# Kernel optimization log

Measured on AMD Instinct MI355X. Metric: run time of the kernel, lower is better.

Reference implementation:

```python
import jax, jax.numpy as jnp
import numpy as np

# Baked genome DAG structure (static per-instance in the original module)
N_IN = 256
LAYER_SIZES = [256, 256, 256, 256, 64]  # 4 hidden layers + output layer
N_OUT = LAYER_SIZES[-1]
N_EVAL = sum(LAYER_SIZES)  # 1088 eval nodes (node_evals)
DEG = 32                   # incoming links per eval node
BATCH = 8192


def setup_inputs() -> dict:
    key = jax.random.key(0)
    kx, kw, kb, kr = jax.random.split(key, 4)
    x = jax.random.normal(kx, (BATCH, N_IN), dtype=jnp.float32)
    # connection weights, node bias, node response (learned genome params)
    w = jax.random.normal(kw, (N_EVAL, DEG), dtype=jnp.float32) * 0.5
    bias = jax.random.normal(kb, (N_EVAL,), dtype=jnp.float32) * 0.1
    response = 1.0 + jax.random.normal(kr, (N_EVAL,), dtype=jnp.float32) * 0.1
    # per-layer source indices: each eval node connects to DEG earlier nodes
    src_rows = []
    offset = N_IN  # number of nodes topologically before current layer
    for li, sz in enumerate(LAYER_SIZES):
        ks = jax.random.fold_in(key, 100 + li)
        src_rows.append(jax.random.randint(ks, (sz, DEG), 0, offset, dtype=jnp.int32))
        offset += sz
    src_idx = jnp.concatenate(src_rows, axis=0)  # [N_EVAL, DEG]
    return {"x": x, "w": w, "bias": bias, "response": response, "src_idx": src_idx}


def reference(x, w, bias, response, src_idx):
    # values: [B, n_nodes_so_far]; starts as the input node values
    values = x
    row = 0
    for sz in LAYER_SIZES:  # small fixed structural loop (topological layers)
        s = src_idx[row:row + sz]                       # [sz, DEG]
        gathered = values[:, s]                         # [B, sz, DEG]
        agg = jnp.einsum('bsd,sd->bs', gathered, w[row:row + sz])  # sum aggregation
        out = jax.nn.relu(bias[row:row + sz] + response[row:row + sz] * agg)
        values = jnp.concatenate([values, out], axis=1)
        row += sz
    return values[:, -N_OUT:]  # [B, N_OUT]
```

## Files before the change

### kernel.cpp

```cpp
#include <hip/hip_runtime.h>

#define N_IN    256
#define N_EVAL  1088
#define TOTALW  1344
#define DEG     32
#define TILE_B  16
#define NTHREADS 256

__device__ __forceinline__ int gbyte(int c, int h) {
    return ((c << 5) + (h << 4)) ^ (int)((((unsigned)c >> 2) & 7u) << 5);
}

__device__ __forceinline__ unsigned int bf16rne2(float lo, float hi) {
    unsigned int ul = __float_as_uint(lo);
    unsigned int uh = __float_as_uint(hi);
    ul = (ul + 0x7fffu + ((ul >> 16) & 1u)) >> 16;
    uh = (uh + 0x7fffu + ((uh >> 16) & 1u)) & 0xffff0000u;
    return ul | uh;
}

__device__ __forceinline__ void fmadw(unsigned int d, float wv, float* acc) {
    acc[0] = fmaf(__uint_as_float(d << 16), wv, acc[0]);
    acc[1] = fmaf(__uint_as_float(d & 0xffff0000u), wv, acc[1]);
}

__device__ __forceinline__ void colacc16(const unsigned int* vals, int c, float wv,
                                         float* acc) {
    const uint4* p = (const uint4*)((const char*)vals + gbyte(c, 0));
    uint4 a = p[0];
    uint4 b = p[1];
    fmadw(a.x, wv, acc + 0);  fmadw(a.y, wv, acc + 2);
    fmadw(a.z, wv, acc + 4);  fmadw(a.w, wv, acc + 6);
    fmadw(b.x, wv, acc + 8);  fmadw(b.y, wv, acc + 10);
    fmadw(b.z, wv, acc + 12); fmadw(b.w, wv, acc + 14);
}

__global__ __launch_bounds__(NTHREADS) void neat_eval(
    const float* __restrict__ x, const float* __restrict__ w,
    const float* __restrict__ bias, const float* __restrict__ resp,
    const int* __restrict__ src, float* __restrict__ out)
{
    __shared__ unsigned int vals[TOTALW * 8];
    const int tid = threadIdx.x;
    const int b0  = blockIdx.x * TILE_B;

    #pragma unroll
    for (int i = 0; i < 2; ++i) {
        int g = tid + i * NTHREADS;
        int c = g & 255;
        int h = g >> 8;
        unsigned int pk[4];
        #pragma unroll
        for (int j = 0; j < 4; ++j) {
            float lo = x[(size_t)(b0 + h * 8 + 2 * j    ) * N_IN + c];
            float hi = x[(size_t)(b0 + h * 8 + 2 * j + 1) * N_IN + c];
            pk[j] = bf16rne2(lo, hi);
        }
        *(uint4*)((char*)vals + gbyte(c, h)) = make_uint4(pk[0], pk[1], pk[2], pk[3]);
    }
    __syncthreads();

    int row = 0, outoff = N_IN;
    #pragma unroll
    for (int li = 0; li < 5; ++li) {
        const int sz = (li < 4) ? 256 : 64;
        for (int n = tid; n < sz; n += NTHREADS) {
            const int gr = row + n;
            const int4*   s4 = (const int4*)(src + (size_t)gr * DEG);
            const float4* w4 = (const float4*)(w   + (size_t)gr * DEG);
            float acc[16];
            #pragma unroll
            for (int i = 0; i < 16; ++i) acc[i] = 0.f;
            #pragma unroll
            for (int k = 0; k < DEG / 4; ++k) {
                int4   i4 = s4[k];
                float4 wv = w4[k];
                colacc16(vals, i4.x, wv.x, acc);
                colacc16(vals, i4.y, wv.y, acc);
                colacc16(vals, i4.z, wv.z, acc);
                colacc16(vals, i4.w, wv.w, acc);
            }
            const float bb = bias[gr], rr = resp[gr];
            unsigned int pk[8];
            #pragma unroll
            for (int j = 0; j < 8; ++j) {
                float lo = fmaxf(fmaf(rr, acc[2 * j    ], bb), 0.f);
                float hi = fmaxf(fmaf(rr, acc[2 * j + 1], bb), 0.f);
                pk[j] = bf16rne2(lo, hi);
            }
            int ob = gbyte(outoff + n, 0);
            *(uint4*)((char*)vals + ob)      = make_uint4(pk[0], pk[1], pk[2], pk[3]);
            *(uint4*)((char*)vals + ob + 16) = make_uint4(pk[4], pk[5], pk[6], pk[7]);
        }
        __syncthreads();
        row += sz; outoff += sz;
    }

    #pragma unroll
    for (int i = 0; i < 4; ++i) {
        int idx = tid + i * NTHREADS;
        int c = idx & 63;
        int b = idx >> 6;
        int col = TOTALW - 64 + c;
        const unsigned int* g =
            (const unsigned int*)((const char*)vals + gbyte(col, b >> 3));
        unsigned int d = g[(b & 7) >> 1];
        float v = (b & 1) ? __uint_as_float(d & 0xffff0000u)
                          : __uint_as_float(d << 16);
        out[(size_t)(b0 + b) * 64 + c] = v;
    }
}

extern "C" void kernel_launch(void* const* d_in, const int* in_sizes, int n_in,
                              void* d_out, int out_size, void* d_ws, size_t ws_size,
                              hipStream_t stream) {
    const float* x    = (const float*)d_in[0];
    const float* w    = (const float*)d_in[1];
    const float* bias = (const float*)d_in[2];
    const float* resp = (const float*)d_in[3];
    const int*   src  = (const int*)d_in[4];
    float* out = (float*)d_out;

    const int batch = in_sizes[0] / N_IN;
    const int grid  = batch / TILE_B;
    neat_eval<<<grid, NTHREADS, 0, stream>>>(x, w, bias, resp, src, out);
}
```

Baseline: 30.32 us.

## Densify sparse genome weights and evaluate layers with bf16 MFMA

Adds a preprocessing kernel that scatters each node's 32 sparse weighted links into a dense bf16 weight matrix laid out in MFMA fragment order, merging duplicate sources. The main kernel then computes each layer as a dense GEMM over all earlier nodes with 16x16x32 bf16 MFMA, 32 batch rows per block and activations kept in swizzled LDS. This replaces scalar gather-FMA work with matrix-core work, at the cost of far more FLOPs (dense over up to 1280 columns), a memset plus an extra kernel launch each call, and reading a roughly 1.5 MB weight buffer. The old scalar kernel remains as a fallback when the workspace is too small.

Result: slower. 57.99 us (+91.3%).

```diff
diff --git a/kernel.cpp b/kernel.cpp
--- a/kernel.cpp
+++ b/kernel.cpp
@@ -1,70 +1,235 @@
 #include <hip/hip_runtime.h>
 
-#define N_IN    256
-#define N_EVAL  1088
-#define TOTALW  1344
-#define DEG     32
-#define TILE_B  16
-#define NTHREADS 256
-
-__device__ __forceinline__ int gbyte(int c, int h) {
-    return ((c << 5) + (h << 4)) ^ (int)((((unsigned)c >> 2) & 7u) << 5);
-}
-
-__device__ __forceinline__ unsigned int bf16rne2(float lo, float hi) {
-    unsigned int ul = __float_as_uint(lo);
-    unsigned int uh = __float_as_uint(hi);
+#define N_IN   256
+#define N_EVAL 1088
+#define TOTALW 1344
+#define DEG    32
+
+typedef __attribute__((ext_vector_type(8))) short short8;
+typedef __attribute__((ext_vector_type(4))) float f32x4;
+typedef unsigned short u16;
+typedef unsigned int   u32;
+
+__device__ __forceinline__ u32 pk2(float lo, float hi) {
+    u32 ul = __float_as_uint(lo);
+    u32 uh = __float_as_uint(hi);
     ul = (ul + 0x7fffu + ((ul >> 16) & 1u)) >> 16;
     uh = (uh + 0x7fffu + ((uh >> 16) & 1u)) & 0xffff0000u;
     return ul | uh;
 }
-
-__device__ __forceinline__ void fmadw(unsigned int d, float wv, float* acc) {
+__device__ __forceinline__ u16 bf1(float v) {
+    u32 u = __float_as_uint(v);
+    return (u16)((u + 0x7fffu + ((u >> 16) & 1u)) >> 16);
+}
+
+__global__ __launch_bounds__(256) void build_m(
+    const int* __restrict__ src, const float* __restrict__ w,
+    u16* __restrict__ B)
+{
+    int gn = blockIdx.x * 256 + threadIdx.x;
+    if (gn >= N_EVAL) return;
+    const int li   = gn >> 8;
+    const int nloc = gn & 255;
+    const int NT   = (li < 4) ? 16 : 4;
+    const int loff[5] = {0, 65536, 196608, 393216, 655360};
+    const int base = loff[li];
+
+    int c[DEG]; float ow[DEG];
+    const int4*   s4 = (const int4*)(src + (size_t)gn * DEG);
+    const float4* w4 = (const float4*)(w   + (size_t)gn * DEG);
+    #pragma unroll
+    for (int k = 0; k < 8; ++k) {
+        int4 ci = s4[k]; float4 wf = w4[k];
+        c[4*k+0]=ci.x; c[4*k+1]=ci.y; c[4*k+2]=ci.z; c[4*k+3]=ci.w;
+        ow[4*k+0]=wf.x; ow[4*k+1]=wf.y; ow[4*k+2]=wf.z; ow[4*k+3]=wf.w;
+    }
+    float acc[DEG]; bool live[DEG];
+    #pragma unroll
+    for (int d = 0; d < DEG; ++d) {
+        float s = 0.f;
+        #pragma unroll
+        for (int d2 = 0; d2 < DEG; ++d2)
+            if (d2 <= d && c[d2] == c[d]) s += ow[d2];
+        acc[d] = s;
+        bool lv = true;
+        #pragma unroll
+        for (int d2 = 0; d2 < DEG; ++d2)
+            if (d2 > d && c[d2] == c[d]) lv = false;
+        live[d] = lv;
+    }
+    const int nt = nloc >> 4, ln = nloc & 15;
+    #pragma unroll
+    for (int d = 0; d < DEG; ++d) {
+        if (!live[d]) continue;
+        int cc = c[d];
+        int kt = cc >> 5, ko = cc & 31;
+        int lane = ((ko >> 3) << 4) | ln;
+        int idx = base + ((kt * NT + nt) * 64 + lane) * 8 + (ko & 7);
+        B[idx] = bf1(acc[d]);
+    }
+}
+
+#define TILE_B 32
+#define RSTRIDE (TOTALW * 2)
+
+__global__ __launch_bounds__(512) void neat_mfma(
+    const float* __restrict__ x, const u16* __restrict__ Bbuf,
+    const float* __restrict__ bias, const float* __restrict__ resp,
+    float* __restrict__ out)
+{
+    __shared__ uint4 ldsq[(TILE_B * RSTRIDE) / 16];
+    char* lds = (char*)ldsq;
+    const int tid  = threadIdx.x;
+    const int b0   = blockIdx.x * TILE_B;
+    const int lane = tid & 63;
+    const int wvid = tid >> 6;
+
+    #pragma unroll
+    for (int i = 0; i < 4; ++i) {
+        int f4 = tid + i * 512;
+        int row = f4 >> 6;
+        int c4  = f4 & 63;
+        float4 xv = ((const float4*)(x + (size_t)(b0 + row) * N_IN))[c4];
+        u32 p0 = pk2(xv.x, xv.y), p1 = pk2(xv.z, xv.w);
+        int byte = row * RSTRIDE + ((c4 * 8) ^ ((row & 7) << 4));
+        *(u32*)(lds + byte)     = p0;
+        *(u32*)(lds + byte + 4) = p1;
+    }
+    __syncthreads();
+
+    const short8* Bf = (const short8*)Bbuf;
+    const int r0  = lane & 15;
+    const int r1  = r0 + 16;
+    const int g16 = (lane >> 4) << 4;
+    const int sw  = (r0 & 7) << 4;
+    const int ab0 = r0 * RSTRIDE;
+    const int ab1 = r1 * RSTRIDE;
+
+    int cbase = N_IN;
+    #pragma unroll
+    for (int li = 0; li < 5; ++li) {
+        const int ktn = (N_IN + li * 256) >> 5;
+        const int loff8[5] = {0, 8192, 24576, 49152, 81920};
+        const int lo8 = loff8[li];
+        const int nbase = cbase - N_IN;
+
+        if (li < 4) {
+            const int NT = 16;
+            const int nt0 = wvid, nt1 = wvid + 8;
+            f32x4 acc00 = {0,0,0,0}, acc01 = {0,0,0,0};
+            f32x4 acc10 = {0,0,0,0}, acc11 = {0,0,0,0};
+            const short8* bp0 = Bf + lo8 + nt0 * 64 + lane;
+            const short8* bp1 = Bf + lo8 + nt1 * 64 + lane;
+            short8 b0v = bp0[0];
+            short8 b1v = bp1[0];
+            for (int kt = 0; kt < ktn; ++kt) {
+                int ktp = (kt + 1 < ktn) ? kt + 1 : kt;
+                short8 nb0 = bp0[ktp * (NT * 64)];
+                short8 nb1 = bp1[ktp * (NT * 64)];
+                int inrow = (kt * 64 + g16) ^ sw;
+                short8 a0 = *(const short8*)(lds + ab0 + inrow);
+                short8 a1 = *(const short8*)(lds + ab1 + inrow);
+                acc00 = __builtin_amdgcn_mfma_f32_16x16x32_bf16(a0, b0v, acc00, 0, 0, 0);
+                acc01 = __builtin_amdgcn_mfma_f32_16x16x32_bf16(a1, b0v, acc01, 0, 0, 0);
+                acc10 = __builtin_amdgcn_mfma_f32_16x16x32_bf16(a0, b1v, acc10, 0, 0, 0);
+                acc11 = __builtin_amdgcn_mfma_f32_16x16x32_bf16(a1, b1v, acc11, 0, 0, 0);
+                b0v = nb0; b1v = nb1;
+            }
+            #pragma unroll
+            for (int t = 0; t < 2; ++t) {
+                int nt = t ? nt1 : nt0;
+                f32x4 aA = t ? acc10 : acc00;
+                f32x4 aB = t ? acc11 : acc01;
+                int gr = nbase + nt * 16 + r0;
+                float bb = bias[gr], rr = resp[gr];
+                int colbyte = (cbase + nt * 16 + r0) * 2;
+                #pragma unroll
+                for (int r = 0; r < 4; ++r) {
+                    int i0 = ((lane >> 4) << 2) + r;
+                    float v0 = fmaxf(fmaf(rr, aA[r], bb), 0.f);
+                    *(u16*)(lds + i0 * RSTRIDE + (colbyte ^ ((i0 & 7) << 4))) = bf1(v0);
+                    int i1 = i0 + 16;
+                    float v1 = fmaxf(fmaf(rr, aB[r], bb), 0.f);
+                    *(u16*)(lds + i1 * RSTRIDE + (colbyte ^ ((i1 & 7) << 4))) = bf1(v1);
+                }
+            }
+            __syncthreads();
+        } else {
+            const int NT = 4;
+            if (wvid < 4) {
+                const int nt0 = wvid;
+                f32x4 acc0 = {0,0,0,0}, acc1 = {0,0,0,0};
+                const short8* bp0 = Bf + lo8 + nt0 * 64 + lane;
+                short8 b0v = bp0[0];
+                for (int kt = 0; kt < ktn; ++kt) {
+                    int ktp = (kt + 1 < ktn) ? kt + 1 : kt;
+                    short8 nb0 = bp0[ktp * (NT * 64)];
+                    int inrow = (kt * 64 + g16) ^ sw;
+                    short8 a0 = *(const short8*)(lds + ab0 + inrow);
+                    short8 a1 = *(const short8*)(lds + ab1 + inrow);
+                    acc0 = __builtin_amdgcn_mfma_f32_16x16x32_bf16(a0, b0v, acc0, 0, 0, 0);
+                    acc1 = __builtin_amdgcn_mfma_f32_16x16x32_bf16(a1, b0v, acc1, 0, 0, 0);
+                    b0v = nb0;
+                }
+                int gr = nbase + nt0 * 16 + r0;
+                float bb = bias[gr], rr = resp[gr];
+                int col = nt0 * 16 + r0;
+                #pragma unroll
+                for (int r = 0; r < 4; ++r) {
+                    int i0 = ((lane >> 4) << 2) + r;
+                    out[(size_t)(b0 + i0) * 64 + col] = fmaxf(fmaf(rr, acc0[r], bb), 0.f);
+                    int i1 = i0 + 16;
+                    out[(size_t)(b0 + i1) * 64 + col] = fmaxf(fmaf(rr, acc1[r], bb), 0.f);
+                }
+            }
+        }
+        cbase += (li < 4) ? 256 : 64;
+    }
+}
+
+#define FTILE_B 16
+__device__ __forceinline__ int gbyte(int c, int h) {
+    return ((c << 5) + (h << 4)) ^ (int)((((unsigned)c >> 2) & 7u) << 5);
+}
+__device__ __forceinline__ void fmadw(u32 d, float wv, float* acc) {
     acc[0] = fmaf(__uint_as_float(d << 16), wv, acc[0]);
     acc[1] = fmaf(__uint_as_float(d & 0xffff0000u), wv, acc[1]);
 }
-
-__device__ __forceinline__ void colacc16(const unsigned int* vals, int c, float wv,
-                                         float* acc) {
+__device__ __forceinline__ void colacc16(const u32* vals, int c, float wv, float* acc) {
     const uint4* p = (const uint4*)((const char*)vals + gbyte(c, 0));
-    uint4 a = p[0];
-    uint4 b = p[1];
+    uint4 a = p[0]; uint4 b = p[1];
     fmadw(a.x, wv, acc + 0);  fmadw(a.y, wv, acc + 2);
     fmadw(a.z, wv, acc + 4);  fmadw(a.w, wv, acc + 6);
     fmadw(b.x, wv, acc + 8);  fmadw(b.y, wv, acc + 10);
     fmadw(b.z, wv, acc + 12); fmadw(b.w, wv, acc + 14);
 }
-
-__global__ __launch_bounds__(NTHREADS) void neat_eval(
+__global__ __launch_bounds__(256) void neat_eval_r4(
     const float* __restrict__ x, const float* __restrict__ w,
     const float* __restrict__ bias, const float* __restrict__ resp,
     const int* __restrict__ src, float* __restrict__ out)
 {
-    __shared__ unsigned int vals[TOTALW * 8];
+    __shared__ u32 vals[TOTALW * 8];
     const int tid = threadIdx.x;
-    const int b0  = blockIdx.x * TILE_B;
-
+    const int b0  = blockIdx.x * FTILE_B;
     #pragma unroll
     for (int i = 0; i < 2; ++i) {
-        int g = tid + i * NTHREADS;
-        int c = g & 255;
-        int h = g >> 8;
-        unsigned int pk[4];
+        int g = tid + i * 256;
+        int c = g & 255, h = g >> 8;
+        u32 pk[4];
         #pragma unroll
         for (int j = 0; j < 4; ++j) {
             float lo = x[(size_t)(b0 + h * 8 + 2 * j    ) * N_IN + c];
             float hi = x[(size_t)(b0 + h * 8 + 2 * j + 1) * N_IN + c];
-            pk[j] = bf16rne2(lo, hi);
+            pk[j] = pk2(lo, hi);
         }
         *(uint4*)((char*)vals + gbyte(c, h)) = make_uint4(pk[0], pk[1], pk[2], pk[3]);
     }
     __syncthreads();
-
     int row = 0, outoff = N_IN;
     #pragma unroll
     for (int li = 0; li < 5; ++li) {
         const int sz = (li < 4) ? 256 : 64;
-        for (int n = tid; n < sz; n += NTHREADS) {
+        for (int n = tid; n < sz; n += 256) {
             const int gr = row + n;
             const int4*   s4 = (const int4*)(src + (size_t)gr * DEG);
             const float4* w4 = (const float4*)(w   + (size_t)gr * DEG);
@@ -73,20 +238,19 @@
             for (int i = 0; i < 16; ++i) acc[i] = 0.f;
             #pragma unroll
             for (int k = 0; k < DEG / 4; ++k) {
-                int4   i4 = s4[k];
-                float4 wv = w4[k];
+                int4 i4 = s4[k]; float4 wv = w4[k];
                 colacc16(vals, i4.x, wv.x, acc);
                 colacc16(vals, i4.y, wv.y, acc);
                 colacc16(vals, i4.z, wv.z, acc);
                 colacc16(vals, i4.w, wv.w, acc);
             }
             const float bb = bias[gr], rr = resp[gr];
-            unsigned int pk[8];
+            u32 pk[8];
             #pragma unroll
             for (int j = 0; j < 8; ++j) {
                 float lo = fmaxf(fmaf(rr, acc[2 * j    ], bb), 0.f);
                 float hi = fmaxf(fmaf(rr, acc[2 * j + 1], bb), 0.f);
-                pk[j] = bf16rne2(lo, hi);
+                pk[j] = pk2(lo, hi);
             }
             int ob = gbyte(outoff + n, 0);
             *(uint4*)((char*)vals + ob)      = make_uint4(pk[0], pk[1], pk[2], pk[3]);
@@ -95,16 +259,13 @@
         __syncthreads();
         row += sz; outoff += sz;
     }
-
     #pragma unroll
     for (int i = 0; i < 4; ++i) {
-        int idx = tid + i * NTHREADS;
-        int c = idx & 63;
-        int b = idx >> 6;
+        int idx = tid + i * 256;
+        int c = idx & 63, b = idx >> 6;
         int col = TOTALW - 64 + c;
-        const unsigned int* g =
-            (const unsigned int*)((const char*)vals + gbyte(col, b >> 3));
-        unsigned int d = g[(b & 7) >> 1];
+        const u32* g = (const u32*)((const char*)vals + gbyte(col, b >> 3));
+        u32 d = g[(b & 7) >> 1];
         float v = (b & 1) ? __uint_as_float(d & 0xffff0000u)
                           : __uint_as_float(d << 16);
         out[(size_t)(b0 + b) * 64 + c] = v;
@@ -122,6 +283,14 @@
     float* out = (float*)d_out;
 
     const int batch = in_sizes[0] / N_IN;
-    const int grid  = batch / TILE_B;
-    neat_eval<<<grid, NTHREADS, 0, stream>>>(x, w, bias, resp, src, out);
-}
+    const size_t need = 737280ull * 2;
+
+    if (ws_size >= need && (batch % TILE_B) == 0) {
+        u16* Bbuf = (u16*)d_ws;
+        hipMemsetAsync(d_ws, 0, need, stream);
+        build_m<<<(N_EVAL + 255) / 256, 256, 0, stream>>>(src, w, Bbuf);
+        neat_mfma<<<batch / TILE_B, 512, 0, stream>>>(x, Bbuf, bias, resp, out);
+    } else {
+        neat_eval_r4<<<batch / FTILE_B, 256, 0, stream>>>(x, w, bias, resp, src, out);
+    }
+}
```
